# Optimization experiments

Measured on AMD Instinct MI355X. Metric: run time of the kernel, lower is better.

## Reference

```python
import jax, jax.numpy as jnp
from jax import lax
import numpy as np

D_MODEL = 512
D_PROJ = 256
PATCH = 4
NL = 8
D_STATE = 16
D_CONV = 4
EXPAND = 2
D_INNER = EXPAND * D_MODEL          # 1024
DT_RANK = (D_MODEL + 15) // 16      # 32
B = 4
SEQ = 1024
NF = 1
EPS = 1e-5


def setup_inputs() -> dict:
    key = jax.random.key(0)
    ks = jax.random.split(key, 12)
    s = 0.02
    def rn(k, shape):
        return jax.random.normal(k, shape, jnp.float32) * s
    A_init = jnp.log(jnp.arange(1, D_STATE + 1, dtype=jnp.float32))  # (n,)
    return {
        "time_series": jax.random.normal(ks[0], (B, SEQ, NF), jnp.float32),
        "mask": jnp.ones((B, SEQ), jnp.int32),
        "emb_w": rn(ks[1], (D_MODEL, PATCH)),
        "emb_b": jnp.zeros((D_MODEL,), jnp.float32),
        "norm_w": jnp.ones((NL, D_MODEL), jnp.float32),
        "in_w": rn(ks[2], (NL, 2, 2 * D_INNER, D_MODEL)),
        "conv_w": rn(ks[3], (NL, 2, D_INNER, D_CONV)),
        "conv_b": jnp.zeros((NL, 2, D_INNER), jnp.float32),
        "xproj_w": rn(ks[4], (NL, 2, DT_RANK + 2 * D_STATE, D_INNER)),
        "dt_w": rn(ks[5], (NL, 2, D_INNER, DT_RANK)),
        "dt_b": jnp.full((NL, 2, D_INNER), float(np.log(np.expm1(0.01))), jnp.float32),
        "A_log": jnp.broadcast_to(A_init, (NL, 2, D_INNER, D_STATE)) + jnp.zeros((NL, 2, D_INNER, D_STATE), jnp.float32),
        "Dp": jnp.ones((NL, 2, D_INNER), jnp.float32),
        "out_w": rn(ks[6], (NL, 2, D_MODEL, D_INNER)),
        "proj_w": rn(ks[7], (PATCH * D_PROJ, D_MODEL)),
        "proj_b": jnp.zeros((PATCH * D_PROJ,), jnp.float32),
    }


def rmsnorm(x, w):
    return x * lax.rsqrt(jnp.mean(x * x, axis=-1, keepdims=True) + EPS) * w


def mamba(x, in_w, conv_w, conv_b, xproj_w, dt_w, dt_b, A_log, Dp, out_w):
    # x: (B, L, D_MODEL)
    Bsz, L, _ = x.shape
    xz = jnp.einsum('bld,ed->ble', x, in_w)                 # (B,L,2*d_inner)
    u, z = jnp.split(xz, 2, axis=-1)                         # each (B,L,d_inner)
    # depthwise causal conv1d along L
    u_t = jnp.transpose(u, (0, 2, 1))                        # (B,d_inner,L)
    u_pad = jnp.pad(u_t, ((0, 0), (0, 0), (D_CONV - 1, 0)))
    conv = lax.conv_general_dilated(
        u_pad, conv_w[:, None, :], window_strides=(1,), padding='VALID',
        feature_group_count=D_INNER, dimension_numbers=('NCH', 'OIH', 'NCH'))
    u = jax.nn.silu(jnp.transpose(conv + conv_b[None, :, None], (0, 2, 1)))  # (B,L,d_inner)
    x_dbl = jnp.einsum('ble,re->blr', u, xproj_w)            # (B,L,dt_rank+2n)
    dt, Bm, C = jnp.split(x_dbl, [DT_RANK, DT_RANK + D_STATE], axis=-1)
    delta = jax.nn.softplus(jnp.einsum('blr,er->ble', dt, dt_w) + dt_b)  # (B,L,d_inner)
    A = -jnp.exp(A_log)                                      # (d_inner,n)

    def step(h, inp):
        d_t, B_t, C_t, u_t = inp                             # (B,e),(B,n),(B,n),(B,e)
        dA = jnp.exp(d_t[..., None] * A)                     # (B,e,n)
        h = dA * h + (d_t * u_t)[..., None] * B_t[:, None, :]
        y = jnp.einsum('ben,bn->be', h, C_t)
        return h, y

    h0 = jnp.zeros((Bsz, D_INNER, D_STATE), x.dtype)
    xs = (jnp.moveaxis(delta, 1, 0), jnp.moveaxis(Bm, 1, 0),
          jnp.moveaxis(C, 1, 0), jnp.moveaxis(u, 1, 0))
    _, ys = lax.scan(step, h0, xs)                           # ys: (L,B,e)
    y = jnp.moveaxis(ys, 0, 1) + u * Dp
    y = y * jax.nn.silu(z)
    return jnp.einsum('ble,de->bld', y, out_w)               # (B,L,D_MODEL)


def reference(time_series, mask, emb_w, emb_b, norm_w, in_w, conv_w, conv_b,
              xproj_w, dt_w, dt_b, A_log, Dp, out_w, proj_w, proj_b):
    Bsz, S, F_ = time_series.shape
    NP = S // PATCH  # S is a multiple of PATCH
    patches = time_series.reshape(Bsz, NP, PATCH, F_)
    patches = jnp.transpose(patches, (0, 3, 1, 2)).reshape(Bsz, F_ * NP, PATCH)
    x = patches @ emb_w.T + emb_b                            # (B, F*NP, D_MODEL)
    for i in range(NL):
        res = x
        xn = rmsnorm(x, norm_w[i])
        yf = mamba(xn, in_w[i, 0], conv_w[i, 0], conv_b[i, 0], xproj_w[i, 0],
                   dt_w[i, 0], dt_b[i, 0], A_log[i, 0], Dp[i, 0], out_w[i, 0])
        yb = mamba(jnp.flip(xn, axis=1), in_w[i, 1], conv_w[i, 1], conv_b[i, 1],
                   xproj_w[i, 1], dt_w[i, 1], dt_b[i, 1], A_log[i, 1], Dp[i, 1], out_w[i, 1])
        x = yf + jnp.flip(yb, axis=1) + res
    proj = x @ proj_w.T + proj_b                             # (B, F*NP, PATCH*D_PROJ)
    le = proj.reshape(Bsz, F_, NP, PATCH, D_PROJ)
    le = jnp.transpose(le, (0, 2, 3, 1, 4)).reshape(Bsz, NP * PATCH, F_, D_PROJ)
    return le[:, :S]
```

## Files before the change

kernel.cpp:

```cpp
#include <hip/hip_runtime.h>
#include <hip/hip_bf16.h>

#define DM 512
#define DI 1024
#define DSTATE 16
#define DTR 32
#define NLAYER 8
#define BS 4
#define LL 256
#define MT 1024
#define DPROJ 256
#define CL 32
#define NCH (LL/CL)

typedef unsigned short u16;
typedef __attribute__((ext_vector_type(8))) short short8;
typedef __attribute__((ext_vector_type(4))) float f32x4;

__device__ __forceinline__ float sigmoidf_(float x){ return 1.f/(1.f+__expf(-x)); }

__device__ __forceinline__ u16 f2bf(float f){
  unsigned u = __float_as_uint(f);
  u = (u + 0x7FFF + ((u>>16)&1)) >> 16;
  return (u16)u;
}
__device__ __forceinline__ float bf2f(u16 v){
  return __uint_as_float(((unsigned)v) << 16);
}

template<int CTRL>
__device__ __forceinline__ float dpp_ror_add(float x){
  int y = __builtin_amdgcn_update_dpp(0, __float_as_int(x), CTRL, 0xF, 0xF, false);
  return x + __int_as_float(y);
}
__device__ __forceinline__ float sum16_dpp(float x){
  x = dpp_ror_add<0x128>(x);
  x = dpp_ror_add<0x124>(x);
  x = dpp_ror_add<0x122>(x);
  x = dpp_ror_add<0x121>(x);
  return x;
}

__global__ __launch_bounds__(256) void embed_k(const float* __restrict__ ts,
    const float* __restrict__ ew, const float* __restrict__ eb, float* __restrict__ x){
  int idx = blockIdx.x*256 + threadIdx.x;
  int m = idx >> 9, d = idx & 511;
  int b = m >> 8, np_ = m & 255;
  const float* t0 = ts + b*1024 + np_*4;
  float acc = eb[d];
  #pragma unroll
  for (int p=0;p<4;p++) acc = fmaf(t0[p], ew[d*4+p], acc);
  x[idx] = acc;
}

__global__ __launch_bounds__(256) void wcastall_k(
    const float* __restrict__ w_in, const float* __restrict__ w_out,
    const float* __restrict__ w_xp, const float* __restrict__ w_pj,
    u16* __restrict__ dst){
  int t = blockIdx.x*256 + threadIdx.x;
  long e4 = (long)t*4;
  const float* src; long o;
  if      (e4 < 16777216) { src = w_in;  o = e4; }
  else if (e4 < 25165824) { src = w_out; o = e4 - 16777216; }
  else if (e4 < 26214400) { src = w_xp;  o = e4 - 25165824; }
  else                    { src = w_pj;  o = e4 - 26214400; }
  float4 v = *(const float4*)(src + o);
  ushort4 r; r.x=f2bf(v.x); r.y=f2bf(v.y); r.z=f2bf(v.z); r.w=f2bf(v.w);
  *(ushort4*)(dst + e4) = r;
}

__global__ __launch_bounds__(256) void rmscomb_k(float* __restrict__ x,
    const float* __restrict__ yout,
    const float* __restrict__ nw, u16* __restrict__ xnbf, u16* __restrict__ xnfbf){
  int m = blockIdx.x, t = threadIdx.x;
  int b = m>>8, l = m&255, mf = (b<<8)+(255-l);
  float2 v = *(const float2*)&x[(long)m*DM + t*2];
  if (yout){
    float2 f = *(const float2*)&yout[(long)m*DM + t*2];
    float2 g = *(const float2*)&yout[(long)MT*DM + (long)mf*DM + t*2];
    v.x += f.x + g.x; v.y += f.y + g.y;
    *(float2*)&x[(long)m*DM + t*2] = v;
  }
  float ss = v.x*v.x + v.y*v.y;
  ss += __shfl_down(ss,32); ss += __shfl_down(ss,16); ss += __shfl_down(ss,8);
  ss += __shfl_down(ss,4);  ss += __shfl_down(ss,2);  ss += __shfl_down(ss,1);
  __shared__ float ps[4];
  if ((t&63)==0) ps[t>>6] = ss;
  __syncthreads();
  float tot = ps[0]+ps[1]+ps[2]+ps[3];
  float rs = rsqrtf(tot*(1.f/DM) + 1e-5f);
  ushort2 o; o.x = f2bf(v.x*rs*nw[t*2]); o.y = f2bf(v.y*rs*nw[t*2+1]);
  *(ushort2*)&xnbf [(long)m *DM + t*2] = o;
  *(ushort2*)&xnfbf[(long)mf*DM + t*2] = o;
}

__global__ __launch_bounds__(256) void combcast_k(const float* __restrict__ x,
    const float* __restrict__ yout, u16* __restrict__ xbf){
  int idx = blockIdx.x*256 + threadIdx.x;
  int m = idx >> 7, c4 = idx & 127;
  int b = m>>8, l = m&255, mf = (b<<8)+(255-l);
  float4 r = ((const float4*)x)[idx];
  float4 f = ((const float4*)yout)[idx];
  float4 g = ((const float4*)(yout + (long)MT*DM))[(long)mf*128 + c4];
  ushort4 o;
  o.x = f2bf(r.x + f.x + g.x); o.y = f2bf(r.y + f.y + g.y);
  o.z = f2bf(r.z + f.z + g.z); o.w = f2bf(r.w + f.w + g.w);
  ((ushort4*)xbf)[idx] = o;
}

template<int BM,int BN,int SPLITK,int EPI>
__global__ __launch_bounds__(256) void mfma_nt(
    const u16* __restrict__ A, int lda, long sA,
    const u16* __restrict__ W, int ldw, long sW,
    const float* __restrict__ bias, u16* __restrict__ G,
    float* __restrict__ C, int ldc, long sC,
    int M, int N, int K)
{
  constexpr int WM = BM/2, WN = BN/2;
  constexpr int MI = WM/16, NI = WN/16;
  int z = blockIdx.z;
  int dir = z / SPLITK, kc = z % SPLITK;
  int Klen = K / SPLITK;
  int kbase = kc * Klen;
  A += (long)dir * sA;
  W += (long)dir * sW;
  if (SPLITK > 1) C += (long)z * M * N; else C += (long)dir * sC;
  if (EPI==4) G += (long)dir * (long)MT*DI;

  __shared__ u16 Al[BM*32];
  __shared__ u16 Wl[BN*32];
  int tid = threadIdx.x;
  int lane = tid & 63;
  int wave = tid >> 6;
  int wm0 = (wave>>1)*WM, wn0 = (wave&1)*WN;
  int m0 = blockIdx.y*BM, n0 = blockIdx.x*BN;
  int l16 = lane>>4, l15 = lane&15;

  f32x4 acc[MI][NI] = {};

  for (int k0=0; k0<Klen; k0+=32){
    #pragma unroll
    for (int it=0; it<BM*4/256; ++it){
      int ch = it*256 + tid;
      int row = ch % BM, kk = ch / BM;
      const u16* g = A + (long)(m0+row)*lda + kbase + k0 + kk*8;
      __builtin_amdgcn_global_load_lds(
          (const __attribute__((address_space(1))) void*)g,
          (__attribute__((address_space(3))) void*)(Al + ch*8), 16, 0, 0);
    }
    #pragma unroll
    for (int it=0; it<BN*4/256; ++it){
      int ch = it*256 + tid;
      int row = ch % BN, kk = ch / BN;
      const u16* g = W + (long)(n0+row)*ldw + kbase + k0 + kk*8;
      __builtin_amdgcn_global_load_lds(
          (const __attribute__((address_space(1))) void*)g,
          (__attribute__((address_space(3))) void*)(Wl + ch*8), 16, 0, 0);
    }
    __syncthreads();
    short8 a[MI], b[NI];
    #pragma unroll
    for (int i=0;i<MI;i++)
      a[i] = *(const short8*)&Al[(l16*BM + wm0 + i*16 + l15)*8];
    #pragma unroll
    for (int j=0;j<NI;j++)
      b[j] = *(const short8*)&Wl[(l16*BN + wn0 + j*16 + l15)*8];
    #pragma unroll
    for (int i=0;i<MI;i++)
      #pragma unroll
      for (int j=0;j<NI;j++)
        acc[i][j] = __builtin_amdgcn_mfma_f32_16x16x32_bf16(a[i], b[j], acc[i][j], 0,0,0);
    __syncthreads();
  }
  #pragma unroll
  for (int i=0;i<MI;i++){
    #pragma unroll
    for (int j=0;j<NI;j++){
      #pragma unroll
      for (int r=0;r<4;r++){
        int m = m0 + wm0 + i*16 + l16*4 + r;
        int n = n0 + wn0 + j*16 + l15;
        float v = acc[i][j][r];
        if (EPI==2){
          v += bias[n];
          int bb = m>>8, np_ = m&255, p = n>>8, dp = n&255;
          C[((long)(bb*1024 + np_*4 + p))*256 + dp] = v;
        } else if (EPI==4){
          if (n < 1024) C[(long)m*1024 + n] = v;
          else          G[(long)m*1024 + (n-1024)] = f2bf(v * sigmoidf_(v));
        } else {
          C[(long)m*ldc + n] = v;
        }
      }
    }
  }
}

__global__ __launch_bounds__(256) void xreduce_k(const float* __restrict__ part,
    float* __restrict__ xdbl){
  int idx = blockIdx.x*256 + threadIdx.x;
  int d = idx >> 16, off = idx & 65535;
  float s = 0.f;
  #pragma unroll
  for (int kc=0; kc<8; ++kc) s += part[((d*8+kc)<<16) + off];
  xdbl[idx] = s;
}

__global__ __launch_bounds__(256) void conv_silu_k(const float* __restrict__ xzu,
    const float* __restrict__ cw, const float* __restrict__ cb,
    u16* __restrict__ ubf){
  int idx = blockIdx.x*256 + threadIdx.x;
  int e = idx & (DI-1);
  int grp = idx >> 10;
  int dir = grp >> 8;
  int b   = (grp >> 6) & 3;
  int l0  = (grp & 63) * 4;
  long dm0 = (long)dir*MT + b*LL + l0;
  const float* w = cw + ((long)dir*DI + e)*4;
  float w0=w[0], w1=w[1], w2=w[2], w3=w[3];
  float bias = cb[dir*DI + e];
  const float* src = xzu + dm0*DI + e;
  float vb[7];
  #pragma unroll
  for (int j=0;j<7;j++){
    int l = l0 - 3 + j;
    vb[j] = (l >= 0) ? src[(long)(j-3)*DI] : 0.f;
  }
  #pragma unroll
  for (int j=0;j<4;j++){
    float acc = bias;
    acc = fmaf(w0, vb[j],   acc);
    acc = fmaf(w1, vb[j+1], acc);
    acc = fmaf(w2, vb[j+2], acc);
    acc = fmaf(w3, vb[j+3], acc);
    float v = acc * sigmoidf_(acc);
    ubf[(dm0+j)*DI + e] = f2bf(v);
  }
}

__global__ __launch_bounds__(256) void scan_k(
    const u16* __restrict__ ubf, const u16* __restrict__ gbf,
    const float* __restrict__ xdbl, const float* __restrict__ dtw,
    const float* __restrict__ dtb, const float* __restrict__ A_log,
    const float* __restrict__ Dp, u16* __restrict__ ygbf)
{
  int t = threadIdx.x;
  int n = t & 15, el = t >> 4;
  int id = blockIdx.x + 64*blockIdx.y + 256*blockIdx.z;
  int xcd = id & 7, slot = id >> 3;
  int ec = xcd*8 + (slot & 7);
  int bd = slot >> 3;
  int b = bd & 3, dir = bd >> 2;

  int e0 = ec*16, e = e0 + el;
  float Av = -__expf(A_log[((long)dir*DI + e)*16 + n]);
  float Dv = Dp[dir*DI + e];
  long mbase = (long)dir*MT + b*LL;
  const u16* up_ = ubf + mbase*DI;
  const u16* gp_ = gbf + mbase*DI;
  const float* xd_ = xdbl + mbase*64;
  u16* yp_ = ygbf + mbase*DI;

  float wrow[32];
  {
    const float* wr = dtw + ((long)dir*DI + e0 + n)*32;
    #pragma unroll
    for (int r4=0;r4<8;r4++) *(float4*)&wrow[r4*4] = *(const float4*)&wr[r4*4];
  }
  float dtbv = dtb[dir*DI + e0 + n];

  __shared__ float sDU[2][16][68];
  __shared__ float sBC[2][16][68];
  __shared__ float sdt[2][32][36];
  __shared__ float sy [32][20];

  float4 xv0, xv1; ushort4 uvv;
  auto load_pre = [&](int c){
    long l0 = (long)c*CL;
    int f0 = t, f1 = t + 256;
    xv0 = *(const float4*)&xd_[(l0 + (f0>>4))*64 + (f0&15)*4];
    xv1 = *(const float4*)&xd_[(l0 + (f1>>4))*64 + (f1&15)*4];
    if (t < 128) uvv = *(const ushort4*)&up_[(l0 + (t>>2))*DI + e0 + (t&3)*4];
  };
  auto write_pre = [&](int buf){
    #pragma unroll
    for (int h_=0; h_<2; ++h_){
      float4 xv = h_ ? xv1 : xv0;
      int f = t + h_*256;
      int row = f>>4, c4 = (f&15)*4;
      if (c4 < 32){
        *(float4*)&sdt[buf][row][c4] = xv;
      } else if (c4 < 48){
        int nb = c4 - 32;
        sBC[buf][nb  ][row*2] = xv.x; sBC[buf][nb+1][row*2] = xv.y;
        sBC[buf][nb+2][row*2] = xv.z; sBC[buf][nb+3][row*2] = xv.w;
      } else {
        int nb = c4 - 48;
        sBC[buf][nb  ][row*2+1] = xv.x; sBC[buf][nb+1][row*2+1] = xv.y;
        sBC[buf][nb+2][row*2+1] = xv.z; sBC[buf][nb+3][row*2+1] = xv.w;
      }
    }
    if (t < 128){
      int l = t>>2, e4 = (t&3)*4;
      sDU[buf][e4  ][l*2+1] = bf2f(uvv.x);
      sDU[buf][e4+1][l*2+1] = bf2f(uvv.y);
      sDU[buf][e4+2][l*2+1] = bf2f(uvv.z);
      sDU[buf][e4+3][l*2+1] = bf2f(uvv.w);
    }
  };

  load_pre(0);
  write_pre(0);
  load_pre(1);
  __syncthreads();

  float h = 0.f;
  int lp = t >> 4;
  for (int c = 0; c < NCH; ++c){
    int cur = c & 1;
    #pragma unroll
    for (int j=0;j<2;j++){
      int l = lp + j*16;
      float acc = dtbv;
      #pragma unroll
      for (int r4=0;r4<8;r4++){
        float4 d4 = *(const float4*)&sdt[cur][l][r4*4];
        acc = fmaf(d4.x, wrow[r4*4],   acc);
        acc = fmaf(d4.y, wrow[r4*4+1], acc);
        acc = fmaf(d4.z, wrow[r4*4+2], acc);
        acc = fmaf(d4.w, wrow[r4*4+3], acc);
      }
      acc = fmaxf(acc, 0.f) + __logf(1.f + __expf(-fabsf(acc)));
      sDU[cur][n][l*2] = acc;
    }
    ushort4 gv;
    if (t < 128) gv = *(const ushort4*)&gp_[((long)c*CL + (t>>2))*DI + e0 + (t&3)*4];
    __syncthreads();

    const float* pDU = &sDU[cur][el][0];
    const float* pBC = &sBC[cur][n][0];
    #pragma unroll
    for (int l2 = 0; l2 < 16; ++l2){
      float4 du = *(const float4*)&pDU[l2*4];
      float4 bc = *(const float4*)&pBC[l2*4];
      {
        float dA = __expf(du.x*Av);
        h = fmaf(dA, h, du.x*du.y*bc.x);
        float yc = sum16_dpp(h*bc.y);
        if (n==0) sy[2*l2][el] = yc + du.y*Dv;
      }
      {
        float dA = __expf(du.z*Av);
        h = fmaf(dA, h, du.z*du.w*bc.z);
        float yc = sum16_dpp(h*bc.w);
        if (n==0) sy[2*l2+1][el] = yc + du.w*Dv;
      }
    }
    __syncthreads();
    if (c+1 < NCH){
      write_pre(cur^1);
      if (c+2 < NCH) load_pre(c+2);
    }
    if (t < 128){
      float4 y4 = *(const float4*)&sy[t>>2][(t&3)*4];
      ushort4 o;
      o.x = f2bf(y4.x * bf2f(gv.x)); o.y = f2bf(y4.y * bf2f(gv.y));
      o.z = f2bf(y4.z * bf2f(gv.z)); o.w = f2bf(y4.w * bf2f(gv.w));
      *(ushort4*)&yp_[((long)c*CL + (t>>2))*DI + e0 + (t&3)*4] = o;
    }
    __syncthreads();
  }
}

extern "C" void kernel_launch(void* const* d_in, const int* in_sizes, int n_in,
                              void* d_out, int out_size, void* d_ws, size_t ws_size,
                              hipStream_t stream){
  const float* ts   = (const float*)d_in[0];
  const float* ew   = (const float*)d_in[2];
  const float* eb   = (const float*)d_in[3];
  const float* nw   = (const float*)d_in[4];
  const float* inw  = (const float*)d_in[5];
  const float* cw   = (const float*)d_in[6];
  const float* cb   = (const float*)d_in[7];
  const float* xpw  = (const float*)d_in[8];
  const float* dtw  = (const float*)d_in[9];
  const float* dtb  = (const float*)d_in[10];
  const float* alog = (const float*)d_in[11];
  const float* dpp  = (const float*)d_in[12];
  const float* outw = (const float*)d_in[13];
  const float* pw   = (const float*)d_in[14];
  const float* pb   = (const float*)d_in[15];
  float* out = (float*)d_out;

  float* ws   = (float*)d_ws;
  float* x    = ws;
  float* xzu  = ws + 524288;
  float* xdbl = ws + 2621440;
  float* yout = ws + 2752512;
  float* xpart= ws + 3801088;
  u16* ub     = (u16*)(ws + 4849664);
  u16* xn_bf  = ub;
  u16* u_bf   = ub + 1048576;
  u16* g_bf   = ub + 3145728;
  u16* yg_bf  = ub + 5242880;
  u16* x_bf   = ub + 7340032;
  u16* wb     = ub + 7864320;
  u16* wb_in  = wb;
  u16* wb_out = wb + 16777216;
  u16* wb_xp  = wb + 25165824;
  u16* wb_pj  = wb + 26214400;

  dim3 blk(256);

  embed_k<<<MT*DM/256, blk, 0, stream>>>(ts, ew, eb, x);
  wcastall_k<<<26112, blk, 0, stream>>>(inw, outw, xpw, pw, wb);

  for (int i=0;i<NLAYER;i++){
    rmscomb_k<<<MT, blk, 0, stream>>>(x, i ? yout : nullptr, nw + i*DM,
        xn_bf, xn_bf + MT*DM);
    mfma_nt<64,128,1,4><<<dim3(16,16,2), blk, 0, stream>>>(
        xn_bf, DM, (long)MT*DM, wb_in + (long)i*2097152, DM, 1048576,
        nullptr, g_bf, xzu, 1024, (long)MT*1024, MT, 2048, DM);
    conv_silu_k<<<2048, blk, 0, stream>>>(xzu, cw + (long)i*2*DI*4, cb + i*2*DI, u_bf);
    mfma_nt<64,64,8,0><<<dim3(1,16,16), blk, 0, stream>>>(
        u_bf, DI, (long)MT*DI, wb_xp + (long)i*131072, DI, 65536,
        nullptr, nullptr, xpart, 64, 0, MT, 64, DI);
    xreduce_k<<<512, blk, 0, stream>>>(xpart, xdbl);
    scan_k<<<dim3(64, BS, 2), blk, 0, stream>>>(u_bf, g_bf, xdbl,
        dtw + (long)i*2*DI*DTR, dtb + (long)i*2*DI,
        alog + (long)i*2*DI*16, dpp + i*2*DI, yg_bf);
    mfma_nt<64,64,1,0><<<dim3(8,16,2), blk, 0, stream>>>(
        yg_bf, DI, (long)MT*DI, wb_out + (long)i*1048576, DI, 524288,
        nullptr, nullptr, yout, DM, (long)MT*DM, MT, DM, DI);
  }
  combcast_k<<<MT*DM/4/256, blk, 0, stream>>>(x, yout, x_bf);
  mfma_nt<64,64,1,2><<<dim3(16,16,1), blk, 0, stream>>>(
      x_bf, DM, 0, wb_pj, DM, 0, pb, nullptr, out, 1024, 0, MT, 1024, DM);
}
```

Baseline: 750.2 us.

## Split selective scan into four parallel sequence segments with carry fixup

The scan kernel now uses 1024 threads per block. Four groups each scan a 64-step segment of the sequence with a zero initial state, while tracking the cumulative decay product. A short cross-segment pass then combines the segment-end states, and a second pass adds the carried-in state contribution to the outputs. The whole 256-step tile is staged in shared memory at once instead of through double-buffered 32-step chunks. The aim is to cut the serial sequence dependency and raise parallelism, at the cost of extra exp work and more shared memory per block.

```diff
diff --git a/kernel.cpp b/kernel.cpp
--- a/kernel.cpp
+++ b/kernel.cpp
@@ -10,8 +10,6 @@
 #define LL 256
 #define MT 1024
 #define DPROJ 256
-#define CL 32
-#define NCH (LL/CL)
 
 typedef unsigned short u16;
 typedef __attribute__((ext_vector_type(8))) short short8;
@@ -238,137 +236,153 @@
   }
 }
 
-__global__ __launch_bounds__(256) void scan_k(
+__global__ __launch_bounds__(1024) void scan_k(
     const u16* __restrict__ ubf, const u16* __restrict__ gbf,
     const float* __restrict__ xdbl, const float* __restrict__ dtw,
     const float* __restrict__ dtb, const float* __restrict__ A_log,
     const float* __restrict__ Dp, u16* __restrict__ ygbf)
 {
   int t = threadIdx.x;
-  int n = t & 15, el = t >> 4;
+  int n  = t & 15;
+  int el = (t >> 4) & 15;
+  int lg = t >> 8;
   int id = blockIdx.x + 64*blockIdx.y + 256*blockIdx.z;
   int xcd = id & 7, slot = id >> 3;
   int ec = xcd*8 + (slot & 7);
   int bd = slot >> 3;
   int b = bd & 3, dir = bd >> 2;
-
-  int e0 = ec*16, e = e0 + el;
-  float Av = -__expf(A_log[((long)dir*DI + e)*16 + n]);
-  float Dv = Dp[dir*DI + e];
+  int e0 = ec*16;
+
   long mbase = (long)dir*MT + b*LL;
   const u16* up_ = ubf + mbase*DI;
   const u16* gp_ = gbf + mbase*DI;
   const float* xd_ = xdbl + mbase*64;
   u16* yp_ = ygbf + mbase*DI;
 
-  float wrow[32];
+  float Av = -__expf(A_log[((long)dir*DI + e0 + el)*16 + n]);
+  float Dv = Dp[dir*DI + e0 + el];
+
+  __shared__ float sDU[16][516];
+  __shared__ float sBC[16][516];
+  __shared__ float sy [256][20];
+  __shared__ float sH [4][16][16];
+  __shared__ float sA [4][16][16];
+  __shared__ float sHin[4][16][16];
+
+  int sl = t >> 2, se4 = (t & 3) * 4;
+  ushort4 gv = *(const ushort4*)&gp_[(long)sl*DI + e0 + se4];
   {
+    ushort4 uv = *(const ushort4*)&up_[(long)sl*DI + e0 + se4];
+    sDU[se4  ][sl*2+1] = bf2f(uv.x);
+    sDU[se4+1][sl*2+1] = bf2f(uv.y);
+    sDU[se4+2][sl*2+1] = bf2f(uv.z);
+    sDU[se4+3][sl*2+1] = bf2f(uv.w);
+  }
+  #pragma unroll
+  for (int h_=0; h_<2; ++h_){
+    int f = t + h_*1024;
+    int row = f >> 3, c4 = (f & 7) * 4;
+    float4 v = *(const float4*)&xd_[(long)row*64 + 32 + c4];
+    if (c4 < 16){
+      int nb = c4;
+      sBC[nb  ][row*2] = v.x; sBC[nb+1][row*2] = v.y;
+      sBC[nb+2][row*2] = v.z; sBC[nb+3][row*2] = v.w;
+    } else {
+      int nb = c4 - 16;
+      sBC[nb  ][row*2+1] = v.x; sBC[nb+1][row*2+1] = v.y;
+      sBC[nb+2][row*2+1] = v.z; sBC[nb+3][row*2+1] = v.w;
+    }
+  }
+  {
+    float wrow[32];
     const float* wr = dtw + ((long)dir*DI + e0 + n)*32;
     #pragma unroll
     for (int r4=0;r4<8;r4++) *(float4*)&wrow[r4*4] = *(const float4*)&wr[r4*4];
-  }
-  float dtbv = dtb[dir*DI + e0 + n];
-
-  __shared__ float sDU[2][16][68];
-  __shared__ float sBC[2][16][68];
-  __shared__ float sdt[2][32][36];
-  __shared__ float sy [32][20];
-
-  float4 xv0, xv1; ushort4 uvv;
-  auto load_pre = [&](int c){
-    long l0 = (long)c*CL;
-    int f0 = t, f1 = t + 256;
-    xv0 = *(const float4*)&xd_[(l0 + (f0>>4))*64 + (f0&15)*4];
-    xv1 = *(const float4*)&xd_[(l0 + (f1>>4))*64 + (f1&15)*4];
-    if (t < 128) uvv = *(const ushort4*)&up_[(l0 + (t>>2))*DI + e0 + (t&3)*4];
-  };
-  auto write_pre = [&](int buf){
-    #pragma unroll
-    for (int h_=0; h_<2; ++h_){
-      float4 xv = h_ ? xv1 : xv0;
-      int f = t + h_*256;
-      int row = f>>4, c4 = (f&15)*4;
-      if (c4 < 32){
-        *(float4*)&sdt[buf][row][c4] = xv;
-      } else if (c4 < 48){
-        int nb = c4 - 32;
-        sBC[buf][nb  ][row*2] = xv.x; sBC[buf][nb+1][row*2] = xv.y;
-        sBC[buf][nb+2][row*2] = xv.z; sBC[buf][nb+3][row*2] = xv.w;
-      } else {
-        int nb = c4 - 48;
-        sBC[buf][nb  ][row*2+1] = xv.x; sBC[buf][nb+1][row*2+1] = xv.y;
-        sBC[buf][nb+2][row*2+1] = xv.z; sBC[buf][nb+3][row*2+1] = xv.w;
-      }
-    }
-    if (t < 128){
-      int l = t>>2, e4 = (t&3)*4;
-      sDU[buf][e4  ][l*2+1] = bf2f(uvv.x);
-      sDU[buf][e4+1][l*2+1] = bf2f(uvv.y);
-      sDU[buf][e4+2][l*2+1] = bf2f(uvv.z);
-      sDU[buf][e4+3][l*2+1] = bf2f(uvv.w);
-    }
-  };
-
-  load_pre(0);
-  write_pre(0);
-  load_pre(1);
-  __syncthreads();
-
-  float h = 0.f;
-  int lp = t >> 4;
-  for (int c = 0; c < NCH; ++c){
-    int cur = c & 1;
-    #pragma unroll
-    for (int j=0;j<2;j++){
-      int l = lp + j*16;
+    float dtbv = dtb[dir*DI + e0 + n];
+    #pragma unroll
+    for (int j=0;j<4;j++){
+      int l = lg*64 + el*4 + j;
+      const float* row = &xd_[(long)l*64];
       float acc = dtbv;
       #pragma unroll
       for (int r4=0;r4<8;r4++){
-        float4 d4 = *(const float4*)&sdt[cur][l][r4*4];
+        float4 d4 = *(const float4*)&row[r4*4];
         acc = fmaf(d4.x, wrow[r4*4],   acc);
         acc = fmaf(d4.y, wrow[r4*4+1], acc);
         acc = fmaf(d4.z, wrow[r4*4+2], acc);
         acc = fmaf(d4.w, wrow[r4*4+3], acc);
       }
       acc = fmaxf(acc, 0.f) + __logf(1.f + __expf(-fabsf(acc)));
-      sDU[cur][n][l*2] = acc;
-    }
-    ushort4 gv;
-    if (t < 128) gv = *(const ushort4*)&gp_[((long)c*CL + (t>>2))*DI + e0 + (t&3)*4];
-    __syncthreads();
-
-    const float* pDU = &sDU[cur][el][0];
-    const float* pBC = &sBC[cur][n][0];
-    #pragma unroll
-    for (int l2 = 0; l2 < 16; ++l2){
+      sDU[n][l*2] = acc;
+    }
+  }
+  __syncthreads();
+
+  const float* pDU = &sDU[el][lg*128];
+  const float* pBC = &sBC[n][lg*128];
+  int lbase = lg*64;
+  float h = 0.f, ap = 1.f;
+  #pragma unroll 8
+  for (int l2 = 0; l2 < 32; ++l2){
+    float4 du = *(const float4*)&pDU[l2*4];
+    float4 bc = *(const float4*)&pBC[l2*4];
+    {
+      float dA = __expf(du.x*Av);
+      h = fmaf(dA, h, du.x*du.y*bc.x);
+      ap *= dA;
+      float yc = sum16_dpp(h*bc.y);
+      if (n==0) sy[lbase+2*l2][el] = yc + du.y*Dv;
+    }
+    {
+      float dA = __expf(du.z*Av);
+      h = fmaf(dA, h, du.z*du.w*bc.z);
+      ap *= dA;
+      float yc = sum16_dpp(h*bc.w);
+      if (n==0) sy[lbase+2*l2+1][el] = yc + du.w*Dv;
+    }
+  }
+  sH[lg][el][n] = h;
+  sA[lg][el][n] = ap;
+  __syncthreads();
+
+  if (t < 256){
+    float hin = 0.f;
+    sHin[0][el][n] = 0.f;
+    #pragma unroll
+    for (int g=1; g<4; ++g){
+      hin = sH[g-1][el][n] + sA[g-1][el][n]*hin;
+      sHin[g][el][n] = hin;
+    }
+  }
+  __syncthreads();
+
+  if (lg > 0){
+    float hin = sHin[lg][el][n];
+    float p = 1.f;
+    #pragma unroll 8
+    for (int l2 = 0; l2 < 32; ++l2){
       float4 du = *(const float4*)&pDU[l2*4];
       float4 bc = *(const float4*)&pBC[l2*4];
       {
-        float dA = __expf(du.x*Av);
-        h = fmaf(dA, h, du.x*du.y*bc.x);
-        float yc = sum16_dpp(h*bc.y);
-        if (n==0) sy[2*l2][el] = yc + du.y*Dv;
+        p *= __expf(du.x*Av);
+        float yc = sum16_dpp(p*hin*bc.y);
+        if (n==0) sy[lbase+2*l2][el] += yc;
       }
       {
-        float dA = __expf(du.z*Av);
-        h = fmaf(dA, h, du.z*du.w*bc.z);
-        float yc = sum16_dpp(h*bc.w);
-        if (n==0) sy[2*l2+1][el] = yc + du.w*Dv;
+        p *= __expf(du.z*Av);
+        float yc = sum16_dpp(p*hin*bc.w);
+        if (n==0) sy[lbase+2*l2+1][el] += yc;
       }
     }
-    __syncthreads();
-    if (c+1 < NCH){
-      write_pre(cur^1);
-      if (c+2 < NCH) load_pre(c+2);
-    }
-    if (t < 128){
-      float4 y4 = *(const float4*)&sy[t>>2][(t&3)*4];
-      ushort4 o;
-      o.x = f2bf(y4.x * bf2f(gv.x)); o.y = f2bf(y4.y * bf2f(gv.y));
-      o.z = f2bf(y4.z * bf2f(gv.z)); o.w = f2bf(y4.w * bf2f(gv.w));
-      *(ushort4*)&yp_[((long)c*CL + (t>>2))*DI + e0 + (t&3)*4] = o;
-    }
-    __syncthreads();
+  }
+  __syncthreads();
+
+  {
+    float4 y4 = *(const float4*)&sy[sl][se4];
+    ushort4 o;
+    o.x = f2bf(y4.x * bf2f(gv.x)); o.y = f2bf(y4.y * bf2f(gv.y));
+    o.z = f2bf(y4.z * bf2f(gv.z)); o.w = f2bf(y4.w * bf2f(gv.w));
+    *(ushort4*)&yp_[(long)sl*DI + e0 + se4] = o;
   }
 }
 
@@ -426,7 +440,7 @@
         u_bf, DI, (long)MT*DI, wb_xp + (long)i*131072, DI, 65536,
         nullptr, nullptr, xpart, 64, 0, MT, 64, DI);
     xreduce_k<<<512, blk, 0, stream>>>(xpart, xdbl);
-    scan_k<<<dim3(64, BS, 2), blk, 0, stream>>>(u_bf, g_bf, xdbl,
+    scan_k<<<dim3(64, BS, 2), dim3(1024), 0, stream>>>(u_bf, g_bf, xdbl,
         dtw + (long)i*2*DI*DTR, dtb + (long)i*2*DI,
         alog + (long)i*2*DI*16, dpp + i*2*DI, yg_bf);
     mfma_nt<64,64,1,0><<<dim3(8,16,2), blk, 0, stream>>>(
```

After: 894.8 us. 1.19x slower.
